# Optimization experiments

Hardware: AMD Instinct MI355X
Metric: run time of the kernel (lower is better)

Reference implementation:

```python
import jax, jax.numpy as jnp
import numpy as np

HEADS = 16
NUM_LANDMARKS = 64
PINV_ITERS = 6
D_MODEL = 1024


def _moore_penrose_pinv(x, num_iters):
    # Newton-Schulz iteration: V <- 0.25*V @ (13I - KV @ (15I - KV @ (7I - KV)))
    m = x.shape[-1]
    I = jnp.eye(m, dtype=x.dtype)
    V = x
    for _ in range(num_iters):
        KV = x @ V  # [..., m, m]
        V = 0.25 * V @ (13.0 * I - KV @ (15.0 * I - KV @ (7.0 * I - KV)))
    return V


def setup_inputs() -> dict:
    key = jax.random.key(0)
    k1, k2, k3 = jax.random.split(key, 3)
    b, n, d = 4, 4096, D_MODEL
    hidden_states = jax.random.normal(k1, (b, n, d), dtype=jnp.float32)
    Wqkv = jax.random.normal(k2, (d, 3 * d), dtype=jnp.float32) * 0.02
    bqkv = jnp.zeros((3 * d,), dtype=jnp.float32)
    Wout = jax.random.normal(k3, (d, d), dtype=jnp.float32) * 0.02
    bout = jnp.zeros((d,), dtype=jnp.float32)
    return {"hidden_states": hidden_states, "Wqkv": Wqkv, "bqkv": bqkv,
            "Wout": Wout, "bout": bout}


def reference(hidden_states, Wqkv, bqkv, Wout, bout):
    b, n, d = hidden_states.shape
    h, m = HEADS, NUM_LANDMARKS
    dh = d // h
    scale = 1.0 / np.sqrt(dh).astype(np.float32)
    # n is a multiple of m by construction, so the torch padding branch is a no-op.
    l = n // m  # tokens per landmark group

    qkv = hidden_states @ Wqkv + bqkv  # [b, n, 3d]
    q, k, v = jnp.split(qkv, 3, axis=-1)

    def to_heads(t):  # [b, n, d] -> [b, h, n, dh]
        return t.reshape(b, n, h, dh).transpose(0, 2, 1, 3)

    q, k, v = to_heads(q), to_heads(k), to_heads(v)
    q = q * scale

    # Landmarks: mean over contiguous groups of l tokens (sum / l in original).
    q_l = q.reshape(b, h, m, l, dh).mean(axis=3)  # [b, h, m, dh]
    k_l = k.reshape(b, h, m, l, dh).mean(axis=3)

    sim1 = jnp.einsum('bhid,bhjd->bhij', q, k_l)    # [b, h, n, m]
    sim2 = jnp.einsum('bhid,bhjd->bhij', q_l, k_l)  # [b, h, m, m]
    sim3 = jnp.einsum('bhid,bhjd->bhij', q_l, k)    # [b, h, m, n]

    attn1 = jax.nn.softmax(sim1, axis=-1)
    attn2 = jax.nn.softmax(sim2, axis=-1)
    attn3 = jax.nn.softmax(sim3, axis=-1)

    attn2_inv = _moore_penrose_pinv(attn2, PINV_ITERS)

    # out = attn1 @ attn2_inv @ (attn3 @ v), cheapest association
    out = attn1 @ (attn2_inv @ (attn3 @ v))  # [b, h, n, dh]
    out = out.transpose(0, 2, 1, 3).reshape(b, n, d)
    out = out @ Wout + bout
    return out
```

## Files before the change

### kernel.cpp

```cpp
#include <hip/hip_runtime.h>
#include <cstdint>

typedef unsigned short u16;
typedef __attribute__((ext_vector_type(8))) short s16x8;
typedef __attribute__((ext_vector_type(4))) float f32x4;

#define NTOK 4096
#define DH   64
#define DM   1024
#define NH   16

static __device__ __forceinline__ float b2f(u16 u){ return __uint_as_float(((unsigned)u)<<16); }
static __device__ __forceinline__ u16 f2b(float f){
  unsigned u = __float_as_uint(f);
  return (u16)((u + 0x7FFFu + ((u>>16)&1u)) >> 16);
}

static __device__ __forceinline__ void gload_lds16(const void* g, void* l) {
  __builtin_amdgcn_global_load_lds(
      (const __attribute__((address_space(1))) unsigned*)(uintptr_t)g,
      (__attribute__((address_space(3))) unsigned*)(uintptr_t)l, 16, 0, 0);
}

static __device__ __forceinline__ s16x8 ld8(const u16* p){ return *(const s16x8*)(const void*)p; }

__global__ __launch_bounds__(256) void k_cvt_xl(const float* __restrict__ hs, u16* __restrict__ Xb,
                                                float* __restrict__ Xl) {
  const int grp = blockIdx.x;
  const int d = blockIdx.y*256 + threadIdx.x;
  const float* p = hs + (long)grp*64*DM + d;
  u16* xo = Xb + (long)grp*64*DM + d;
  float s = 0.f;
  #pragma unroll 8
  for (int i = 0; i < 64; ++i) {
    const float v = p[(long)i*DM];
    s += v;
    xo[(long)i*DM] = f2b(v);
  }
  Xl[(long)grp*DM + d] = s * (1.0f/64.0f);
}

__global__ __launch_bounds__(256) void k_cvt_t(const float* __restrict__ in, u16* __restrict__ out, int R, int C) {
  __shared__ float tile[64][65];
  const int tc = blockIdx.x, tr = blockIdx.y;
  const int t = threadIdx.x, cx = t & 63, ry = t >> 6;
  #pragma unroll
  for (int p = 0; p < 16; ++p) {
    const int row = p*4 + ry;
    tile[row][cx] = in[(long)(tr*64 + row)*C + tc*64 + cx];
  }
  __syncthreads();
  #pragma unroll
  for (int p = 0; p < 16; ++p) {
    const int orow = p*4 + ry;
    out[(long)(tc*64 + orow)*R + tr*64 + cx] = f2b(tile[cx][orow]);
  }
}

__global__ __launch_bounds__(256) void k_lproj2(const float* __restrict__ Xl, const float* __restrict__ Wqkv,
                                                float* __restrict__ psum) {
  __shared__ __align__(16) float Xs[32][68];
  const int t = threadIdx.x;
  const int wcol = blockIdx.x*256 + t;
  const int r0 = blockIdx.y*32;
  const int kbase = blockIdx.z*128;
  float acc[32];
  #pragma unroll
  for (int r = 0; r < 32; ++r) acc[r] = 0.f;
  for (int k0 = kbase; k0 < kbase + 128; k0 += 64) {
    __syncthreads();
    for (int idx = t; idx < 2048; idx += 256)
      Xs[idx>>6][idx&63] = Xl[(long)(r0 + (idx>>6))*DM + k0 + (idx&63)];
    __syncthreads();
    for (int kk = 0; kk < 64; kk += 4) {
      f32x4 wv;
      #pragma unroll
      for (int j = 0; j < 4; ++j) wv[j] = Wqkv[(long)(k0+kk+j)*3072 + wcol];
      #pragma unroll
      for (int r = 0; r < 32; ++r) {
        const f32x4 xv = *(const f32x4*)&Xs[r][kk];
        acc[r] += xv[0]*wv[0] + xv[1]*wv[1] + xv[2]*wv[2] + xv[3]*wv[3];
      }
    }
  }
  float* po = psum + ((long)blockIdx.z*256 + r0)*2048 + wcol;
  #pragma unroll
  for (int r = 0; r < 32; ++r) po[(long)r*2048] = acc[r];
}

__global__ __launch_bounds__(256) void k_lreduce(const float* __restrict__ psum, const float* __restrict__ bqkv,
                                                 float* __restrict__ qlf, float* __restrict__ klf,
                                                 u16* __restrict__ qlb, u16* __restrict__ klb) {
  const long idx = (long)blockIdx.x*256 + threadIdx.x;
  const int row = (int)(idx >> 11), col = (int)(idx & 2047);
  float s = 0.f;
  #pragma unroll
  for (int z = 0; z < 8; ++z) s += psum[((long)z*256 + row)*2048 + col];
  const int isq = (col < 1024) ? 1 : 0;
  float val = s + bqkv[col];
  if (isq) val *= 0.125f;
  const int b = row >> 6, lm = row & 63;
  const int c2 = col & 1023, h = c2 >> 6, dh = c2 & 63;
  const long o = (((long)b*NH + h)*64 + lm)*64 + dh;
  if (isq) { qlf[o] = val; qlb[o] = f2b(val); }
  else     { klf[o] = val; klb[o] = f2b(val); }
}

template<int EPI>
__global__ __launch_bounds__(512, 2) void k_gemm256(
    const u16* __restrict__ A, const u16* __restrict__ Bt, const float* __restrict__ bias,
    int N, float* __restrict__ outF, u16* __restrict__ outQ, u16* __restrict__ outK, u16* __restrict__ outV)
{
  __shared__ __align__(16) u16 lds[4*16384];
  const int K = 1024;
  const int t = threadIdx.x;
  const int lane = t & 63;
  const int wid = t >> 6;
  const int c = lane & 15, g = lane >> 4;
  const int wm = wid >> 2, wn = wid & 3;
  const int fid = blockIdx.y*64 + blockIdx.x;
  const int nbx = ((fid & 7) << 3) | ((fid >> 3) & 7);
  const int nby = fid >> 6;
  const long arow0 = (long)nbx * 256;
  const long brow0 = (long)nby * 256;
  char* ldsb = (char*)lds;

  const int srow = t >> 2;
  const int schunk = (t & 3) ^ ((srow >> 1) & 3);
  const u16* gA0 = A  + (arow0 + srow)*K       + schunk*8;
  const u16* gA1 = A  + (arow0 + 128 + srow)*K + schunk*8;
  const u16* gB0 = Bt + (brow0 + srow)*K       + schunk*8;
  const u16* gB1 = Bt + (brow0 + 128 + srow)*K + schunk*8;
  const int dstoff = t*16;

#define STAGE_A(kt) { char* bse = ldsb + ((kt)&3)*32768; \
    gload_lds16(gA0 + (kt)*32, bse + dstoff); \
    gload_lds16(gA1 + (kt)*32, bse + 8192 + dstoff); }
#define STAGE_B(kt) { char* bse = ldsb + ((kt)&3)*32768 + 16384; \
    gload_lds16(gB0 + (kt)*32, bse + dstoff); \
    gload_lds16(gB1 + (kt)*32, bse + 8192 + dstoff); }

  const int gs = g ^ ((c >> 1) & 3);
  int aoff[2][4], boff[4];
  #pragma unroll
  for (int mi = 0; mi < 4; ++mi) {
    aoff[0][mi] = (0*128 + wm*64 + mi*16 + c)*64 + gs*16;
    aoff[1][mi] = (1*128 + wm*64 + mi*16 + c)*64 + gs*16;
    boff[mi]    = 16384 + (wn*64 + mi*16 + c)*64 + gs*16;
  }

  f32x4 acc0[4][4] = {};
  f32x4 acc1[4][4] = {};

  STAGE_A(0); STAGE_B(0); STAGE_A(1); STAGE_B(1); STAGE_A(2); STAGE_B(2);
  asm volatile("s_waitcnt vmcnt(8)" ::: "memory");
  __builtin_amdgcn_s_barrier();

  s16x8 af[4], bfr[4], af2[4];
  #pragma unroll
  for (int mi = 0; mi < 4; ++mi) af[mi]  = *(const s16x8*)(ldsb + aoff[0][mi]);
  #pragma unroll
  for (int ni = 0; ni < 4; ++ni) bfr[ni] = *(const s16x8*)(ldsb + boff[ni]);

  for (int kt = 0; kt < 32; ++kt) {
    char* buf  = ldsb + (kt&3)*32768;
    char* bufn = ldsb + ((kt+1)&3)*32768;
    if (kt + 3 < 32) { STAGE_A(kt+3) STAGE_B(kt+3) }
    asm volatile("s_waitcnt lgkmcnt(0)" ::: "memory");
    __builtin_amdgcn_sched_barrier(0);
    #pragma unroll
    for (int mi = 0; mi < 4; ++mi) af2[mi] = *(const s16x8*)(buf + aoff[1][mi]);
    __builtin_amdgcn_sched_barrier(0);
    __builtin_amdgcn_s_setprio(1);
    #pragma unroll
    for (int mi = 0; mi < 4; ++mi)
      #pragma unroll
      for (int ni = 0; ni < 4; ++ni)
        acc0[mi][ni] = __builtin_amdgcn_mfma_f32_16x16x32_bf16(af[mi], bfr[ni], acc0[mi][ni], 0, 0, 0);
    __builtin_amdgcn_s_setprio(0);
    asm volatile("s_waitcnt lgkmcnt(0)" ::: "memory");
    __builtin_amdgcn_sched_barrier(0);
    if (kt <= 28)      { asm volatile("s_waitcnt vmcnt(8)" ::: "memory"); }
    else if (kt == 29) { asm volatile("s_waitcnt vmcnt(4)" ::: "memory"); }
    else if (kt == 30) { asm volatile("s_waitcnt vmcnt(0)" ::: "memory"); }
    if (kt < 31) __builtin_amdgcn_s_barrier();
    s16x8 nf[4], nb[4];
    if (kt < 31) {
      #pragma unroll
      for (int mi = 0; mi < 4; ++mi) nf[mi] = *(const s16x8*)(bufn + aoff[0][mi]);
      #pragma unroll
      for (int ni = 0; ni < 4; ++ni) nb[ni] = *(const s16x8*)(bufn + boff[ni]);
    }
    __builtin_amdgcn_sched_barrier(0);
    __builtin_amdgcn_s_setprio(1);
    #pragma unroll
    for (int mi = 0; mi < 4; ++mi)
      #pragma unroll
      for (int ni = 0; ni < 4; ++ni)
        acc1[mi][ni] = __builtin_amdgcn_mfma_f32_16x16x32_bf16(af2[mi], bfr[ni], acc1[mi][ni], 0, 0, 0);
    __builtin_amdgcn_s_setprio(0);
    if (kt < 31) {
      #pragma unroll
      for (int mi = 0; mi < 4; ++mi) { af[mi] = nf[mi]; bfr[mi] = nb[mi]; }
    }
  }
#undef STAGE_A
#undef STAGE_B

  if (EPI == 0) {
    const int tensor = (int)(brow0 >> 10);
    u16* dst = (tensor == 0) ? outQ : (tensor == 1) ? outK : outV;
    const float mul = (tensor == 0) ? 0.125f : 1.0f;
    #pragma unroll
    for (int ph = 0; ph < 2; ++ph)
      #pragma unroll
      for (int mi = 0; mi < 4; ++mi) {
        const int rowb = ph*128 + wm*64 + mi*16 + g*4;
        #pragma unroll
        for (int ni = 0; ni < 4; ++ni) {
          const long gcol = brow0 + wn*64 + ni*16 + c;
          const int c2 = (int)(gcol & 1023);
          const int head = c2 >> 6, dh = c2 & 63;
          const float bv = bias[gcol];
          const f32x4 a = ph ? acc1[mi][ni] : acc0[mi][ni];
          #pragma unroll
          for (int r = 0; r < 4; ++r) {
            const long grow = arow0 + rowb + r;
            const int b = (int)(grow >> 12), tok = (int)(grow & 4095);
            dst[(((long)b*NH + head)*NTOK + tok)*DH + dh] = f2b((a[r] + bv)*mul);
          }
        }
      }
  } else {
    #pragma unroll
    for (int ph = 0; ph < 2; ++ph)
      #pragma unroll
      for (int mi = 0; mi < 4; ++mi) {
        const int rowb = ph*128 + wm*64 + mi*16 + g*4;
        #pragma unroll
        for (int ni = 0; ni < 4; ++ni) {
          const long gcol = brow0 + wn*64 + ni*16 + c;
          const float bv = bias[gcol];
          const f32x4 a = ph ? acc1[mi][ni] : acc0[mi][ni];
          #pragma unroll
          for (int r = 0; r < 4; ++r) {
            const long grow = arow0 + rowb + r;
            outF[grow*N + gcol] = a[r] + bv;
          }
        }
      }
  }
}

__global__ __launch_bounds__(256) void k_vtrans(const u16* __restrict__ v, u16* __restrict__ vt) {
  __shared__ u16 tile[64][65];
  const int bh = blockIdx.x >> 6, tt = blockIdx.x & 63;
  const int t = threadIdx.x, cx = t & 63, ry = t >> 6;
  const u16* vp = v + ((long)bh*NTOK + tt*64)*DH;
  #pragma unroll
  for (int p = 0; p < 16; ++p) { const int row = p*4 + ry; tile[row][cx] = vp[row*DH + cx]; }
  __syncthreads();
  u16* op = vt + (long)bh*DH*NTOK + tt*64;
  #pragma unroll
  for (int p = 0; p < 16; ++p) { const int orow = p*4 + ry; op[(long)orow*NTOK + cx] = tile[cx][orow]; }
}

#define PST 68
static __device__ __forceinline__ void mm_nn8(const float* A, const float* B, float* C, int t) {
  const int lane = t & 63, j0 = (t >> 6) << 3;
  float acc[8];
  #pragma unroll
  for (int j = 0; j < 8; ++j) acc[j] = 0.f;
  for (int k = 0; k < 64; k += 4) {
    const f32x4 a4 = *(const f32x4*)&A[lane*PST + k];
    #pragma unroll
    for (int dk = 0; dk < 4; ++dk) {
      const float a = a4[dk];
      const float* br = &B[(k + dk)*PST + j0];
      const f32x4 b0 = *(const f32x4*)(br);
      const f32x4 b1 = *(const f32x4*)(br + 4);
      #pragma unroll
      for (int qq = 0; qq < 4; ++qq) { acc[qq] += a*b0[qq]; acc[4+qq] += a*b1[qq]; }
    }
  }
  #pragma unroll
  for (int j = 0; j < 8; ++j) C[lane*PST + j0 + j] = acc[j];
}
static __device__ __forceinline__ void mm_nt8(const float* A, const float* B, float* C, int t) {
  const int lane = t & 63, j0 = (t >> 6) << 3;
  float acc[8];
  #pragma unroll
  for (int j = 0; j < 8; ++j) acc[j] = 0.f;
  for (int k = 0; k < 64; k += 4) {
    const f32x4 a4 = *(const f32x4*)&A[lane*PST + k];
    #pragma unroll
    for (int jj = 0; jj < 8; ++jj) {
      const f32x4 b4 = *(const f32x4*)&B[(j0 + jj)*PST + k];
      acc[jj] += a4[0]*b4[0] + a4[1]*b4[1] + a4[2]*b4[2] + a4[3]*b4[3];
    }
  }
  #pragma unroll
  for (int j = 0; j < 8; ++j) C[lane*PST + j0 + j] = acc[j];
}

__global__ __launch_bounds__(512) void k_pinv(const float* __restrict__ qlf, const float* __restrict__ klf,
                                              float* __restrict__ a2inv) {
  __shared__ __align__(16) float Xb[64*PST];
  __shared__ __align__(16) float Vb[64*PST];
  __shared__ __align__(16) float T1[64*PST];
  __shared__ __align__(16) float T2[64*PST];
  __shared__ __align__(16) float T3[64*PST];
  const int bh = blockIdx.x, t = threadIdx.x;
  const float* ql = qlf + (long)bh*4096;
  const float* kl = klf + (long)bh*4096;
  for (int i = t; i < 4096; i += 512) { T1[(i>>6)*PST + (i&63)] = ql[i]; T2[(i>>6)*PST + (i&63)] = kl[i]; }
  __syncthreads();
  mm_nt8(T1, T2, Xb, t);
  __syncthreads();
  if (t < 64) {
    float mx = -1e30f;
    for (int j = 0; j < 64; ++j) mx = fmaxf(mx, Xb[t*PST + j]);
    float s = 0.f;
    for (int j = 0; j < 64; ++j) { const float e = expf(Xb[t*PST + j] - mx); Xb[t*PST + j] = e; s += e; }
    const float inv = 1.0f/s;
    for (int j = 0; j < 64; ++j) Xb[t*PST + j] *= inv;
  }
  __syncthreads();
  for (int i = t; i < 4096; i += 512) { const int r = i>>6, cc = i&63; Vb[r*PST+cc] = Xb[r*PST+cc]; }
  __syncthreads();
  for (int it = 0; it < 6; ++it) {
    mm_nn8(Xb, Vb, T1, t);  __syncthreads();
    for (int i = t; i < 4096; i += 512) { const int r=i>>6, cc=i&63; T2[r*PST+cc] = (r==cc?7.0f:0.0f) - T1[r*PST+cc]; }
    __syncthreads();
    mm_nn8(T1, T2, T3, t);  __syncthreads();
    for (int i = t; i < 4096; i += 512) { const int r=i>>6, cc=i&63; T2[r*PST+cc] = (r==cc?15.0f:0.0f) - T3[r*PST+cc]; }
    __syncthreads();
    mm_nn8(T1, T2, T3, t);  __syncthreads();
    for (int i = t; i < 4096; i += 512) { const int r=i>>6, cc=i&63; T2[r*PST+cc] = (r==cc?13.0f:0.0f) - T3[r*PST+cc]; }
    __syncthreads();
    mm_nn8(Vb, T2, T3, t);  __syncthreads();
    for (int i = t; i < 4096; i += 512) { const int r=i>>6, cc=i&63; Vb[r*PST+cc] = 0.25f*T3[r*PST+cc]; }
    __syncthreads();
  }
  for (int i = t; i < 4096; i += 512) a2inv[(long)bh*4096 + i] = Vb[(i>>6)*PST + (i&63)];
}

__global__ __launch_bounds__(256) void k_attn3v_p(const u16* __restrict__ qlb, const u16* __restrict__ kk,
                                                  const u16* __restrict__ vt,
                                                  float* __restrict__ zp, float* __restrict__ sp) {
  __shared__ __align__(16) float Zl[4][64][64];
  __shared__ float Sl[4][64];
  __shared__ __align__(16) u16 Pl[4][64][40];
  const int bh = blockIdx.x >> 2, qt = blockIdx.x & 3;
  const int t = threadIdx.x, w = t >> 6, lane = t & 63;
  const int c = lane & 15, g = lane >> 4;

  s16x8 aq[4][2];
  const u16* qlp = qlb + (long)bh*4096;
  #pragma unroll
  for (int mi = 0; mi < 4; ++mi)
    #pragma unroll
    for (int ks = 0; ks < 2; ++ks)
      aq[mi][ks] = ld8(qlp + (mi*16 + c)*64 + ks*32 + g*8);

  f32x4 zacc[4][4] = {};
  float sl[4][4] = {};
  const u16* kp = kk + (long)bh*NTOK*DH;
  const u16* vp = vt + (long)bh*DH*NTOK;
  char* pbase = (char*)&Pl[w][0][0];
  const int tok00 = qt*1024 + w*256;

  for (int it = 0; it < 8; ++it) {
    const int t0 = tok00 + it*32;
    f32x4 sacc[4][2] = {};
    s16x8 kb[2][2];
    #pragma unroll
    for (int cg = 0; cg < 2; ++cg)
      #pragma unroll
      for (int ks = 0; ks < 2; ++ks)
        kb[cg][ks] = ld8(kp + (long)(t0 + cg*16 + c)*64 + ks*32 + g*8);
    #pragma unroll
    for (int cg = 0; cg < 2; ++cg)
      #pragma unroll
      for (int ks = 0; ks < 2; ++ks)
        #pragma unroll
        for (int mi = 0; mi < 4; ++mi)
          sacc[mi][cg] = __builtin_amdgcn_mfma_f32_16x16x32_bf16(aq[mi][ks], kb[cg][ks], sacc[mi][cg], 0, 0, 0);
    #pragma unroll
    for (int mi = 0; mi < 4; ++mi)
      #pragma unroll
      for (int r = 0; r < 4; ++r) {
        const int row = mi*16 + g*4 + r;
        const float p0 = __expf(sacc[mi][0][r]);
        const float p1 = __expf(sacc[mi][1][r]);
        sl[mi][r] += p0 + p1;
        char* base = pbase + row*80;
        *(u16*)(base + c*2)      = f2b(p0);
        *(u16*)(base + 32 + c*2) = f2b(p1);
      }
    s16x8 pa[4];
    #pragma unroll
    for (int mi = 0; mi < 4; ++mi) pa[mi] = *(const s16x8*)(pbase + (mi*16 + c)*80 + g*16);
    #pragma unroll
    for (int ni = 0; ni < 4; ++ni) {
      const s16x8 vb = ld8(vp + (long)(ni*16 + c)*NTOK + t0 + g*8);
      #pragma unroll
      for (int mi = 0; mi < 4; ++mi)
        zacc[mi][ni] = __builtin_amdgcn_mfma_f32_16x16x32_bf16(pa[mi], vb, zacc[mi][ni], 0, 0, 0);
    }
  }
  #pragma unroll
  for (int mi = 0; mi < 4; ++mi)
    #pragma unroll
    for (int r = 0; r < 4; ++r) {
      float s = sl[mi][r];
      s += __shfl_xor(s, 1); s += __shfl_xor(s, 2); s += __shfl_xor(s, 4); s += __shfl_xor(s, 8);
      sl[mi][r] = s;
    }
  #pragma unroll
  for (int mi = 0; mi < 4; ++mi)
    #pragma unroll
    for (int ni = 0; ni < 4; ++ni)
      #pragma unroll
      for (int r = 0; r < 4; ++r)
        Zl[w][mi*16 + g*4 + r][ni*16 + c] = zacc[mi][ni][r];
  if (c == 0)
    #pragma unroll
    for (int mi = 0; mi < 4; ++mi)
      #pragma unroll
      for (int r = 0; r < 4; ++r)
        Sl[w][mi*16 + g*4 + r] = sl[mi][r];
  __syncthreads();
  float* zpp = zp + (long)blockIdx.x*4096;
  for (int i = t; i < 4096; i += 256) {
    const int row = i >> 6, dh = i & 63;
    zpp[i] = Zl[0][row][dh] + Zl[1][row][dh] + Zl[2][row][dh] + Zl[3][row][dh];
  }
  if (t < 64) sp[(long)blockIdx.x*64 + t] = Sl[0][t] + Sl[1][t] + Sl[2][t] + Sl[3][t];
}

__global__ __launch_bounds__(512) void k_w2(const float* __restrict__ a2inv,
                                            const float* __restrict__ zp, const float* __restrict__ sp,
                                            u16* __restrict__ w2t) {
  __shared__ __align__(16) float Ai[64*PST];
  __shared__ __align__(16) float Zi[64*PST];
  __shared__ __align__(16) float Ci[64*PST];
  __shared__ float Ss[64];
  const int bh = blockIdx.x, t = threadIdx.x;
  if (t < 64) {
    float ss = 0.f;
    #pragma unroll
    for (int qt = 0; qt < 4; ++qt) ss += sp[(long)(bh*4 + qt)*64 + t];
    Ss[t] = 1.0f / ss;
  }
  for (int i = t; i < 4096; i += 512)
    Ai[(i>>6)*PST + (i&63)] = a2inv[(long)bh*4096 + i];
  __syncthreads();
  for (int i = t; i < 4096; i += 512) {
    float zs = 0.f;
    #pragma unroll
    for (int qt = 0; qt < 4; ++qt) zs += zp[((long)(bh*4 + qt))*4096 + i];
    Zi[(i>>6)*PST + (i&63)] = zs * Ss[i>>6];
  }
  __syncthreads();
  mm_nn8(Ai, Zi, Ci, t);
  __syncthreads();
  for (int i = t; i < 4096; i += 512) { const int r = i>>6, cc = i&63; w2t[(long)bh*4096 + cc*64 + r] = f2b(Ci[r*PST + cc]); }
}

#define P1ST 144
__global__ __launch_bounds__(256) void k_attn1(const u16* __restrict__ q, const u16* __restrict__ klb,
                                               const u16* __restrict__ w2t, u16* __restrict__ ao) {
  __shared__ __align__(16) u16 Pl[4][64][72];
  const int bx = blockIdx.x, bh = bx >> 4, tt = bx & 15;
  const int b = bh >> 4, h = bh & 15;
  const int t = threadIdx.x, w = t >> 6, lane = t & 63;
  const int c = lane & 15, g = lane >> 4;
  const int tok0 = tt*256 + w*64;
  const u16* qp  = q + ((long)bh*NTOK + tok0)*DH;
  const u16* klp = klb + (long)bh*4096;
  const u16* wp  = w2t + (long)bh*4096;
  char* pbase = (char*)&Pl[w][0][0];

  s16x8 aq[4][2], kb[4][2], wb[4][2];
  #pragma unroll
  for (int i = 0; i < 4; ++i)
    #pragma unroll
    for (int ks = 0; ks < 2; ++ks) {
      aq[i][ks] = ld8(qp + (long)(i*16 + c)*DH + ks*32 + g*8);
      kb[i][ks] = ld8(klp + (i*16 + c)*64 + ks*32 + g*8);
      wb[i][ks] = ld8(wp  + (i*16 + c)*64 + ks*32 + g*8);
    }
  f32x4 sacc[4][4] = {};
  #pragma unroll
  for (int ks = 0; ks < 2; ++ks)
    #pragma unroll
    for (int mi = 0; mi < 4; ++mi)
      #pragma unroll
      for (int ni = 0; ni < 4; ++ni)
        sacc[mi][ni] = __builtin_amdgcn_mfma_f32_16x16x32_bf16(aq[mi][ks], kb[ni][ks], sacc[mi][ni], 0, 0, 0);

  float rs[4][4];
  #pragma unroll
  for (int mi = 0; mi < 4; ++mi)
    #pragma unroll
    for (int r = 0; r < 4; ++r) {
      const int row = mi*16 + g*4 + r;
      char* base = pbase + row*P1ST;
      float ssum = 0.f;
      #pragma unroll
      for (int ni = 0; ni < 4; ++ni) {
        const float p = __expf(sacc[mi][ni][r]);
        ssum += p;
        *(u16*)(base + (ni*16 + c)*2) = f2b(p);
      }
      ssum += __shfl_xor(ssum, 1); ssum += __shfl_xor(ssum, 2);
      ssum += __shfl_xor(ssum, 4); ssum += __shfl_xor(ssum, 8);
      rs[mi][r] = ssum;
    }
  __builtin_amdgcn_s_barrier();
  s16x8 pa[4][2];
  #pragma unroll
  for (int mi = 0; mi < 4; ++mi)
    #pragma unroll
    for (int ks = 0; ks < 2; ++ks)
      pa[mi][ks] = *(const s16x8*)(pbase + (mi*16 + c)*P1ST + ks*64 + g*16);
  f32x4 oacc[4][4] = {};
  #pragma unroll
  for (int ks = 0; ks < 2; ++ks)
    #pragma unroll
    for (int mi = 0; mi < 4; ++mi)
      #pragma unroll
      for (int ni = 0; ni < 4; ++ni)
        oacc[mi][ni] = __builtin_amdgcn_mfma_f32_16x16x32_bf16(pa[mi][ks], wb[ni][ks], oacc[mi][ni], 0, 0, 0);

  u16* op = ao + (long)b*NTOK*DM + (long)h*64;
  #pragma unroll
  for (int mi = 0; mi < 4; ++mi)
    #pragma unroll
    for (int r = 0; r < 4; ++r) {
      const int tok = tok0 + mi*16 + g*4 + r;
      const float inv = 1.0f / rs[mi][r];
      #pragma unroll
      for (int ni = 0; ni < 4; ++ni)
        op[(long)tok*DM + ni*16 + c] = f2b(oacc[mi][ni][r] * inv);
    }
}

extern "C" void kernel_launch(void* const* d_in, const int* in_sizes, int n_in,
                              void* d_out, int out_size, void* d_ws, size_t ws_size,
                              hipStream_t stream) {
  const float* hs   = (const float*)d_in[0];
  const float* Wqkv = (const float*)d_in[1];
  const float* bqkv = (const float*)d_in[2];
  const float* Wout = (const float*)d_in[3];
  const float* bout = (const float*)d_in[4];
  float* out = (float*)d_out;
  char* w = (char*)d_ws;

  u16*  Xb    = (u16*)(w);
  float* zp   = (float*)(w);
  float* sp   = (float*)(w + 4194304L);
  u16*  WqkvT = (u16*)(w + 33554432L);
  u16*  WoutT = (u16*)(w + 39845888L);
  u16*  q     = (u16*)(w + 41943040L);
  float* psum = (float*)(w + 41943040L);
  u16*  k     = (u16*)(w + 75497472L);
  u16*  v     = (u16*)(w + 109051904L);
  u16*  vt    = (u16*)(w + 142606336L);
  float* Xl   = (float*)(w + 142606336L);
  float* qlf  = (float*)(w + 176160768L);
  float* klf  = (float*)(w + 177209344L);
  u16*  qlb   = (u16*)(w + 178257920L);
  u16*  klb   = (u16*)(w + 178782208L);
  float* a2i  = (float*)(w + 179306496L);
  u16*  w2t   = (u16*)(w + 181403648L);
  u16*  ao    = (u16*)(w + 181927936L);

  k_cvt_xl<<<dim3(256,4), 256, 0, stream>>>(hs, Xb, Xl);
  k_cvt_t<<<dim3(48,16), 256, 0, stream>>>(Wqkv, WqkvT, 1024, 3072);
  k_cvt_t<<<dim3(16,16), 256, 0, stream>>>(Wout, WoutT, 1024, 1024);
  k_lproj2<<<dim3(8,8,8), 256, 0, stream>>>(Xl, Wqkv, psum);
  k_lreduce<<<2048, 256, 0, stream>>>(psum, bqkv, qlf, klf, qlb, klb);
  k_gemm256<0><<<dim3(64,12), 512, 0, stream>>>(Xb, WqkvT, bqkv, 3072, nullptr, q, k, v);
  k_vtrans<<<4096, 256, 0, stream>>>(v, vt);
  k_pinv<<<64, 512, 0, stream>>>(qlf, klf, a2i);
  k_attn3v_p<<<256, 256, 0, stream>>>(qlb, k, vt, zp, sp);
  k_w2<<<64, 512, 0, stream>>>(a2i, zp, sp, w2t);
  k_attn1<<<1024, 256, 0, stream>>>(q, klb, w2t, ao);
  k_gemm256<1><<<dim3(64,4), 512, 0, stream>>>(ao, WoutT, bout, 1024, out, nullptr, nullptr, nullptr);
}
```

Before: 367.6 us.

## Fuse V transpose into QKV GEMM, restage GEMM loop, widen pinv/attn3 parallelism

```diff
diff --git a/kernel.cpp b/kernel.cpp
--- a/kernel.cpp
+++ b/kernel.cpp
@@ -133,12 +133,10 @@
   const u16* gB1 = Bt + (brow0 + 128 + srow)*K + schunk*8;
   const int dstoff = t*16;
 
-#define STAGE_A(kt) { char* bse = ldsb + ((kt)&3)*32768; \
-    gload_lds16(gA0 + (kt)*32, bse + dstoff); \
-    gload_lds16(gA1 + (kt)*32, bse + 8192 + dstoff); }
-#define STAGE_B(kt) { char* bse = ldsb + ((kt)&3)*32768 + 16384; \
-    gload_lds16(gB0 + (kt)*32, bse + dstoff); \
-    gload_lds16(gB1 + (kt)*32, bse + 8192 + dstoff); }
+#define GL_A0(kt) gload_lds16(gA0 + (kt)*32, ldsb + ((kt)&3)*32768 + dstoff);
+#define GL_A1(kt) gload_lds16(gA1 + (kt)*32, ldsb + ((kt)&3)*32768 + 8192 + dstoff);
+#define GL_B0(kt) gload_lds16(gB0 + (kt)*32, ldsb + ((kt)&3)*32768 + 16384 + dstoff);
+#define GL_B1(kt) gload_lds16(gB1 + (kt)*32, ldsb + ((kt)&3)*32768 + 24576 + dstoff);
 
   const int gs = g ^ ((c >> 1) & 3);
   int aoff[2][4], boff[4];
@@ -152,85 +150,129 @@
   f32x4 acc0[4][4] = {};
   f32x4 acc1[4][4] = {};
 
-  STAGE_A(0); STAGE_B(0); STAGE_A(1); STAGE_B(1); STAGE_A(2); STAGE_B(2);
+  GL_A0(0) GL_A1(0) GL_B0(0) GL_B1(0)
+  GL_A0(1) GL_A1(1) GL_B0(1) GL_B1(1)
+  GL_A0(2) GL_A1(2) GL_B0(2) GL_B1(2)
   asm volatile("s_waitcnt vmcnt(8)" ::: "memory");
   __builtin_amdgcn_s_barrier();
 
-  s16x8 af[4], bfr[4], af2[4];
-  #pragma unroll
-  for (int mi = 0; mi < 4; ++mi) af[mi]  = *(const s16x8*)(ldsb + aoff[0][mi]);
-  #pragma unroll
-  for (int ni = 0; ni < 4; ++ni) bfr[ni] = *(const s16x8*)(ldsb + boff[ni]);
-
   for (int kt = 0; kt < 32; ++kt) {
-    char* buf  = ldsb + (kt&3)*32768;
-    char* bufn = ldsb + ((kt+1)&3)*32768;
-    if (kt + 3 < 32) { STAGE_A(kt+3) STAGE_B(kt+3) }
+    char* buf = ldsb + (kt&3)*32768;
+    s16x8 fa0, fa1, fb[4];
+    if (kt + 3 < 32) GL_A0(kt+3)
+    fa0 = *(const s16x8*)(buf + aoff[0][0]);
+    fa1 = *(const s16x8*)(buf + aoff[0][1]);
+    #pragma unroll
+    for (int ni = 0; ni < 4; ++ni) fb[ni] = *(const s16x8*)(buf + boff[ni]);
     asm volatile("s_waitcnt lgkmcnt(0)" ::: "memory");
     __builtin_amdgcn_sched_barrier(0);
-    #pragma unroll
-    for (int mi = 0; mi < 4; ++mi) af2[mi] = *(const s16x8*)(buf + aoff[1][mi]);
+    __builtin_amdgcn_s_setprio(1);
+    #pragma unroll
+    for (int ni = 0; ni < 4; ++ni) acc0[0][ni] = __builtin_amdgcn_mfma_f32_16x16x32_bf16(fa0, fb[ni], acc0[0][ni], 0, 0, 0);
+    #pragma unroll
+    for (int ni = 0; ni < 4; ++ni) acc0[1][ni] = __builtin_amdgcn_mfma_f32_16x16x32_bf16(fa1, fb[ni], acc0[1][ni], 0, 0, 0);
+    __builtin_amdgcn_s_setprio(0);
+    if (kt + 3 < 32) GL_A1(kt+3)
+    fa0 = *(const s16x8*)(buf + aoff[0][2]);
+    fa1 = *(const s16x8*)(buf + aoff[0][3]);
+    asm volatile("s_waitcnt lgkmcnt(0)" ::: "memory");
     __builtin_amdgcn_sched_barrier(0);
     __builtin_amdgcn_s_setprio(1);
     #pragma unroll
-    for (int mi = 0; mi < 4; ++mi)
-      #pragma unroll
-      for (int ni = 0; ni < 4; ++ni)
-        acc0[mi][ni] = __builtin_amdgcn_mfma_f32_16x16x32_bf16(af[mi], bfr[ni], acc0[mi][ni], 0, 0, 0);
+    for (int ni = 0; ni < 4; ++ni) acc0[2][ni] = __builtin_amdgcn_mfma_f32_16x16x32_bf16(fa0, fb[ni], acc0[2][ni], 0, 0, 0);
+    #pragma unroll
+    for (int ni = 0; ni < 4; ++ni) acc0[3][ni] = __builtin_amdgcn_mfma_f32_16x16x32_bf16(fa1, fb[ni], acc0[3][ni], 0, 0, 0);
     __builtin_amdgcn_s_setprio(0);
+    if (kt + 3 < 32) GL_B0(kt+3)
+    fa0 = *(const s16x8*)(buf + aoff[1][0]);
+    fa1 = *(const s16x8*)(buf + aoff[1][1]);
     asm volatile("s_waitcnt lgkmcnt(0)" ::: "memory");
     __builtin_amdgcn_sched_barrier(0);
+    __builtin_amdgcn_s_setprio(1);
+    #pragma unroll
+    for (int ni = 0; ni < 4; ++ni) acc1[0][ni] = __builtin_amdgcn_mfma_f32_16x16x32_bf16(fa0, fb[ni], acc1[0][ni], 0, 0, 0);
+    #pragma unroll
+    for (int ni = 0; ni < 4; ++ni) acc1[1][ni] = __builtin_amdgcn_mfma_f32_16x16x32_bf16(fa1, fb[ni], acc1[1][ni], 0, 0, 0);
+    __builtin_amdgcn_s_setprio(0);
+    if (kt + 3 < 32) GL_B1(kt+3)
+    fa0 = *(const s16x8*)(buf + aoff[1][2]);
+    fa1 = *(const s16x8*)(buf + aoff[1][3]);
+    asm volatile("s_waitcnt lgkmcnt(0)" ::: "memory");
+    __builtin_amdgcn_sched_barrier(0);
+    __builtin_amdgcn_s_setprio(1);
+    #pragma unroll
+    for (int ni = 0; ni < 4; ++ni) acc1[2][ni] = __builtin_amdgcn_mfma_f32_16x16x32_bf16(fa0, fb[ni], acc1[2][ni], 0, 0, 0);
+    #pragma unroll
+    for (int ni = 0; ni < 4; ++ni) acc1[3][ni] = __builtin_amdgcn_mfma_f32_16x16x32_bf16(fa1, fb[ni], acc1[3][ni], 0, 0, 0);
+    __builtin_amdgcn_s_setprio(0);
     if (kt <= 28)      { asm volatile("s_waitcnt vmcnt(8)" ::: "memory"); }
     else if (kt == 29) { asm volatile("s_waitcnt vmcnt(4)" ::: "memory"); }
     else if (kt == 30) { asm volatile("s_waitcnt vmcnt(0)" ::: "memory"); }
-    if (kt < 31) __builtin_amdgcn_s_barrier();
-    s16x8 nf[4], nb[4];
-    if (kt < 31) {
-      #pragma unroll
-      for (int mi = 0; mi < 4; ++mi) nf[mi] = *(const s16x8*)(bufn + aoff[0][mi]);
-      #pragma unroll
-      for (int ni = 0; ni < 4; ++ni) nb[ni] = *(const s16x8*)(bufn + boff[ni]);
-    }
-    __builtin_amdgcn_sched_barrier(0);
-    __builtin_amdgcn_s_setprio(1);
-    #pragma unroll
-    for (int mi = 0; mi < 4; ++mi)
-      #pragma unroll
-      for (int ni = 0; ni < 4; ++ni)
-        acc1[mi][ni] = __builtin_amdgcn_mfma_f32_16x16x32_bf16(af2[mi], bfr[ni], acc1[mi][ni], 0, 0, 0);
-    __builtin_amdgcn_s_setprio(0);
-    if (kt < 31) {
-      #pragma unroll
-      for (int mi = 0; mi < 4; ++mi) { af[mi] = nf[mi]; bfr[mi] = nb[mi]; }
-    }
-  }
-#undef STAGE_A
-#undef STAGE_B
+    __builtin_amdgcn_s_barrier();
+  }
+#undef GL_A0
+#undef GL_A1
+#undef GL_B0
+#undef GL_B1
 
   if (EPI == 0) {
     const int tensor = (int)(brow0 >> 10);
-    u16* dst = (tensor == 0) ? outQ : (tensor == 1) ? outK : outV;
-    const float mul = (tensor == 0) ? 0.125f : 1.0f;
-    #pragma unroll
-    for (int ph = 0; ph < 2; ++ph)
-      #pragma unroll
-      for (int mi = 0; mi < 4; ++mi) {
-        const int rowb = ph*128 + wm*64 + mi*16 + g*4;
+    if (tensor == 2) {
+      __syncthreads();
+      u16* wlds = lds + wid*4224;
+      const int hbase = (int)((brow0 + wn*64) & 1023);
+      const int head = hbase >> 6;
+      #pragma unroll
+      for (int ph = 0; ph < 2; ++ph) {
+        const long grow0 = arow0 + ph*128 + wm*64;
+        const int b = (int)(grow0 >> 12), tok0r = (int)(grow0 & 4095);
         #pragma unroll
-        for (int ni = 0; ni < 4; ++ni) {
-          const long gcol = brow0 + wn*64 + ni*16 + c;
-          const int c2 = (int)(gcol & 1023);
-          const int head = c2 >> 6, dh = c2 & 63;
-          const float bv = bias[gcol];
-          const f32x4 a = ph ? acc1[mi][ni] : acc0[mi][ni];
+        for (int mi = 0; mi < 4; ++mi)
           #pragma unroll
-          for (int r = 0; r < 4; ++r) {
-            const long grow = arow0 + rowb + r;
-            const int b = (int)(grow >> 12), tok = (int)(grow & 4095);
-            dst[(((long)b*NH + head)*NTOK + tok)*DH + dh] = f2b((a[r] + bv)*mul);
+          for (int ni = 0; ni < 4; ++ni) {
+            const float bv = bias[brow0 + wn*64 + ni*16 + c];
+            const f32x4 a = ph ? acc1[mi][ni] : acc0[mi][ni];
+            #pragma unroll
+            for (int r = 0; r < 4; ++r)
+              wlds[(mi*16 + g*4 + r)*66 + ni*16 + c] = f2b(a[r] + bv);
+          }
+        asm volatile("s_waitcnt lgkmcnt(0)" ::: "memory");
+        u16* vbase = outV + (((long)b*NH + head)*DH)*NTOK + tok0r;
+        #pragma unroll
+        for (int j = 0; j < 8; ++j) {
+          const int d = j*8 + (lane >> 3);
+          const int tk = (lane & 7)*8;
+          s16x8 vv;
+          #pragma unroll
+          for (int s2 = 0; s2 < 8; ++s2) vv[s2] = (short)wlds[(tk + s2)*66 + d];
+          *(s16x8*)(vbase + (long)d*NTOK + tk) = vv;
+        }
+        asm volatile("s_waitcnt lgkmcnt(0)" ::: "memory");
+      }
+    } else {
+      u16* dst = (tensor == 0) ? outQ : outK;
+      const float mul = (tensor == 0) ? 0.125f : 1.0f;
+      #pragma unroll
+      for (int ph = 0; ph < 2; ++ph)
+        #pragma unroll
+        for (int mi = 0; mi < 4; ++mi) {
+          const int rowb = ph*128 + wm*64 + mi*16 + g*4;
+          #pragma unroll
+          for (int ni = 0; ni < 4; ++ni) {
+            const long gcol = brow0 + wn*64 + ni*16 + c;
+            const int c2 = (int)(gcol & 1023);
+            const int head = c2 >> 6, dh = c2 & 63;
+            const float bv = bias[gcol];
+            const f32x4 a = ph ? acc1[mi][ni] : acc0[mi][ni];
+            #pragma unroll
+            for (int r = 0; r < 4; ++r) {
+              const long grow = arow0 + rowb + r;
+              const int b = (int)(grow >> 12), tok = (int)(grow & 4095);
+              dst[(((long)b*NH + head)*NTOK + tok)*DH + dh] = f2b((a[r] + bv)*mul);
+            }
           }
         }
-      }
+    }
   } else {
     #pragma unroll
     for (int ph = 0; ph < 2; ++ph)
@@ -252,59 +294,39 @@
   }
 }
 
-__global__ __launch_bounds__(256) void k_vtrans(const u16* __restrict__ v, u16* __restrict__ vt) {
-  __shared__ u16 tile[64][65];
-  const int bh = blockIdx.x >> 6, tt = blockIdx.x & 63;
-  const int t = threadIdx.x, cx = t & 63, ry = t >> 6;
-  const u16* vp = v + ((long)bh*NTOK + tt*64)*DH;
-  #pragma unroll
-  for (int p = 0; p < 16; ++p) { const int row = p*4 + ry; tile[row][cx] = vp[row*DH + cx]; }
-  __syncthreads();
-  u16* op = vt + (long)bh*DH*NTOK + tt*64;
-  #pragma unroll
-  for (int p = 0; p < 16; ++p) { const int orow = p*4 + ry; op[(long)orow*NTOK + cx] = tile[cx][orow]; }
-}
-
 #define PST 68
-static __device__ __forceinline__ void mm_nn8(const float* A, const float* B, float* C, int t) {
-  const int lane = t & 63, j0 = (t >> 6) << 3;
-  float acc[8];
-  #pragma unroll
-  for (int j = 0; j < 8; ++j) acc[j] = 0.f;
+static __device__ __forceinline__ void mm_nn4(const float* A, const float* B, float* C, int t) {
+  const int lane = t & 63, j0 = (t >> 6) << 2;
+  float acc[4] = {0.f, 0.f, 0.f, 0.f};
   for (int k = 0; k < 64; k += 4) {
     const f32x4 a4 = *(const f32x4*)&A[lane*PST + k];
     #pragma unroll
     for (int dk = 0; dk < 4; ++dk) {
-      const float a = a4[dk];
-      const float* br = &B[(k + dk)*PST + j0];
-      const f32x4 b0 = *(const f32x4*)(br);
-      const f32x4 b1 = *(const f32x4*)(br + 4);
-      #pragma unroll
-      for (int qq = 0; qq < 4; ++qq) { acc[qq] += a*b0[qq]; acc[4+qq] += a*b1[qq]; }
-    }
-  }
-  #pragma unroll
-  for (int j = 0; j < 8; ++j) C[lane*PST + j0 + j] = acc[j];
-}
-static __device__ __forceinline__ void mm_nt8(const float* A, const float* B, float* C, int t) {
-  const int lane = t & 63, j0 = (t >> 6) << 3;
-  float acc[8];
-  #pragma unroll
-  for (int j = 0; j < 8; ++j) acc[j] = 0.f;
+      const f32x4 b0 = *(const f32x4*)&B[(k + dk)*PST + j0];
+      #pragma unroll
+      for (int q = 0; q < 4; ++q) acc[q] += a4[dk]*b0[q];
+    }
+  }
+  #pragma unroll
+  for (int j = 0; j < 4; ++j) C[lane*PST + j0 + j] = acc[j];
+}
+static __device__ __forceinline__ void mm_nt4(const float* A, const float* B, float* C, int t) {
+  const int lane = t & 63, j0 = (t >> 6) << 2;
+  float acc[4] = {0.f, 0.f, 0.f, 0.f};
   for (int k = 0; k < 64; k += 4) {
     const f32x4 a4 = *(const f32x4*)&A[lane*PST + k];
     #pragma unroll
-    for (int jj = 0; jj < 8; ++jj) {
+    for (int jj = 0; jj < 4; ++jj) {
       const f32x4 b4 = *(const f32x4*)&B[(j0 + jj)*PST + k];
       acc[jj] += a4[0]*b4[0] + a4[1]*b4[1] + a4[2]*b4[2] + a4[3]*b4[3];
     }
   }
   #pragma unroll
-  for (int j = 0; j < 8; ++j) C[lane*PST + j0 + j] = acc[j];
-}
-
-__global__ __launch_bounds__(512) void k_pinv(const float* __restrict__ qlf, const float* __restrict__ klf,
-                                              float* __restrict__ a2inv) {
+  for (int j = 0; j < 4; ++j) C[lane*PST + j0 + j] = acc[j];
+}
+
+__global__ __launch_bounds__(1024) void k_pinv(const float* __restrict__ qlf, const float* __restrict__ klf,
+                                               float* __restrict__ a2inv) {
   __shared__ __align__(16) float Xb[64*PST];
   __shared__ __align__(16) float Vb[64*PST];
   __shared__ __align__(16) float T1[64*PST];
@@ -313,9 +335,9 @@
   const int bh = blockIdx.x, t = threadIdx.x;
   const float* ql = qlf + (long)bh*4096;
   const float* kl = klf + (long)bh*4096;
-  for (int i = t; i < 4096; i += 512) { T1[(i>>6)*PST + (i&63)] = ql[i]; T2[(i>>6)*PST + (i&63)] = kl[i]; }
-  __syncthreads();
-  mm_nt8(T1, T2, Xb, t);
+  for (int i = t; i < 4096; i += 1024) { T1[(i>>6)*PST + (i&63)] = ql[i]; T2[(i>>6)*PST + (i&63)] = kl[i]; }
+  __syncthreads();
+  mm_nt4(T1, T2, Xb, t);
   __syncthreads();
   if (t < 64) {
     float mx = -1e30f;
@@ -326,23 +348,23 @@
     for (int j = 0; j < 64; ++j) Xb[t*PST + j] *= inv;
   }
   __syncthreads();
-  for (int i = t; i < 4096; i += 512) { const int r = i>>6, cc = i&63; Vb[r*PST+cc] = Xb[r*PST+cc]; }
+  for (int i = t; i < 4096; i += 1024) { const int r = i>>6, cc = i&63; Vb[r*PST+cc] = Xb[r*PST+cc]; }
   __syncthreads();
   for (int it = 0; it < 6; ++it) {
-    mm_nn8(Xb, Vb, T1, t);  __syncthreads();
-    for (int i = t; i < 4096; i += 512) { const int r=i>>6, cc=i&63; T2[r*PST+cc] = (r==cc?7.0f:0.0f) - T1[r*PST+cc]; }
+    mm_nn4(Xb, Vb, T1, t);  __syncthreads();
+    for (int i = t; i < 4096; i += 1024) { const int r=i>>6, cc=i&63; T2[r*PST+cc] = (r==cc?7.0f:0.0f) - T1[r*PST+cc]; }
     __syncthreads();
-    mm_nn8(T1, T2, T3, t);  __syncthreads();
-    for (int i = t; i < 4096; i += 512) { const int r=i>>6, cc=i&63; T2[r*PST+cc] = (r==cc?15.0f:0.0f) - T3[r*PST+cc]; }
+    mm_nn4(T1, T2, T3, t);  __syncthreads();
+    for (int i = t; i < 4096; i += 1024) { const int r=i>>6, cc=i&63; T2[r*PST+cc] = (r==cc?15.0f:0.0f) - T3[r*PST+cc]; }
     __syncthreads();
-    mm_nn8(T1, T2, T3, t);  __syncthreads();
-    for (int i = t; i < 4096; i += 512) { const int r=i>>6, cc=i&63; T2[r*PST+cc] = (r==cc?13.0f:0.0f) - T3[r*PST+cc]; }
+    mm_nn4(T1, T2, T3, t);  __syncthreads();
+    for (int i = t; i < 4096; i += 1024) { const int r=i>>6, cc=i&63; T2[r*PST+cc] = (r==cc?13.0f:0.0f) - T3[r*PST+cc]; }
     __syncthreads();
-    mm_nn8(Vb, T2, T3, t);  __syncthreads();
-    for (int i = t; i < 4096; i += 512) { const int r=i>>6, cc=i&63; Vb[r*PST+cc] = 0.25f*T3[r*PST+cc]; }
+    mm_nn4(Vb, T2, T3, t);  __syncthreads();
+    for (int i = t; i < 4096; i += 1024) { const int r=i>>6, cc=i&63; Vb[r*PST+cc] = 0.25f*T3[r*PST+cc]; }
     __syncthreads();
   }
-  for (int i = t; i < 4096; i += 512) a2inv[(long)bh*4096 + i] = Vb[(i>>6)*PST + (i&63)];
+  for (int i = t; i < 4096; i += 1024) a2inv[(long)bh*4096 + i] = Vb[(i>>6)*PST + (i&63)];
 }
 
 __global__ __launch_bounds__(256) void k_attn3v_p(const u16* __restrict__ qlb, const u16* __restrict__ kk,
@@ -351,7 +373,7 @@
   __shared__ __align__(16) float Zl[4][64][64];
   __shared__ float Sl[4][64];
   __shared__ __align__(16) u16 Pl[4][64][40];
-  const int bh = blockIdx.x >> 2, qt = blockIdx.x & 3;
+  const int bh = blockIdx.x >> 3, qt = blockIdx.x & 7;
   const int t = threadIdx.x, w = t >> 6, lane = t & 63;
   const int c = lane & 15, g = lane >> 4;
 
@@ -368,9 +390,9 @@
   const u16* kp = kk + (long)bh*NTOK*DH;
   const u16* vp = vt + (long)bh*DH*NTOK;
   char* pbase = (char*)&Pl[w][0][0];
-  const int tok00 = qt*1024 + w*256;
-
-  for (int it = 0; it < 8; ++it) {
+  const int tok00 = qt*512 + w*128;
+
+  for (int it = 0; it < 4; ++it) {
     const int t0 = tok00 + it*32;
     f32x4 sacc[4][2] = {};
     s16x8 kb[2][2];
@@ -439,9 +461,9 @@
   if (t < 64) sp[(long)blockIdx.x*64 + t] = Sl[0][t] + Sl[1][t] + Sl[2][t] + Sl[3][t];
 }
 
-__global__ __launch_bounds__(512) void k_w2(const float* __restrict__ a2inv,
-                                            const float* __restrict__ zp, const float* __restrict__ sp,
-                                            u16* __restrict__ w2t) {
+__global__ __launch_bounds__(1024) void k_w2(const float* __restrict__ a2inv,
+                                             const float* __restrict__ zp, const float* __restrict__ sp,
+                                             u16* __restrict__ w2t) {
   __shared__ __align__(16) float Ai[64*PST];
   __shared__ __align__(16) float Zi[64*PST];
   __shared__ __align__(16) float Ci[64*PST];
@@ -450,22 +472,22 @@
   if (t < 64) {
     float ss = 0.f;
     #pragma unroll
-    for (int qt = 0; qt < 4; ++qt) ss += sp[(long)(bh*4 + qt)*64 + t];
+    for (int qt = 0; qt < 8; ++qt) ss += sp[(long)(bh*8 + qt)*64 + t];
     Ss[t] = 1.0f / ss;
   }
-  for (int i = t; i < 4096; i += 512)
+  for (int i = t; i < 4096; i += 1024)
     Ai[(i>>6)*PST + (i&63)] = a2inv[(long)bh*4096 + i];
   __syncthreads();
-  for (int i = t; i < 4096; i += 512) {
+  for (int i = t; i < 4096; i += 1024) {
     float zs = 0.f;
     #pragma unroll
-    for (int qt = 0; qt < 4; ++qt) zs += zp[((long)(bh*4 + qt))*4096 + i];
+    for (int qt = 0; qt < 8; ++qt) zs += zp[((long)(bh*8 + qt))*4096 + i];
     Zi[(i>>6)*PST + (i&63)] = zs * Ss[i>>6];
   }
   __syncthreads();
-  mm_nn8(Ai, Zi, Ci, t);
-  __syncthreads();
-  for (int i = t; i < 4096; i += 512) { const int r = i>>6, cc = i&63; w2t[(long)bh*4096 + cc*64 + r] = f2b(Ci[r*PST + cc]); }
+  mm_nn4(Ai, Zi, Ci, t);
+  __syncthreads();
+  for (int i = t; i < 4096; i += 1024) { const int r = i>>6, cc = i&63; w2t[(long)bh*4096 + cc*64 + r] = f2b(Ci[r*PST + cc]); }
 }
 
 #define P1ST 144
@@ -560,15 +582,14 @@
 
   u16*  Xb    = (u16*)(w);
   float* zp   = (float*)(w);
-  float* sp   = (float*)(w + 4194304L);
+  float* sp   = (float*)(w + 8388608L);
   u16*  WqkvT = (u16*)(w + 33554432L);
   u16*  WoutT = (u16*)(w + 39845888L);
   u16*  q     = (u16*)(w + 41943040L);
   float* psum = (float*)(w + 41943040L);
   u16*  k     = (u16*)(w + 75497472L);
-  u16*  v     = (u16*)(w + 109051904L);
   u16*  vt    = (u16*)(w + 142606336L);
-  float* Xl   = (float*)(w + 142606336L);
+  float* Xl   = (float*)(w + 109051904L);
   float* qlf  = (float*)(w + 176160768L);
   float* klf  = (float*)(w + 177209344L);
   u16*  qlb   = (u16*)(w + 178257920L);
@@ -582,11 +603,10 @@
   k_cvt_t<<<dim3(16,16), 256, 0, stream>>>(Wout, WoutT, 1024, 1024);
   k_lproj2<<<dim3(8,8,8), 256, 0, stream>>>(Xl, Wqkv, psum);
   k_lreduce<<<2048, 256, 0, stream>>>(psum, bqkv, qlf, klf, qlb, klb);
-  k_gemm256<0><<<dim3(64,12), 512, 0, stream>>>(Xb, WqkvT, bqkv, 3072, nullptr, q, k, v);
-  k_vtrans<<<4096, 256, 0, stream>>>(v, vt);
-  k_pinv<<<64, 512, 0, stream>>>(qlf, klf, a2i);
-  k_attn3v_p<<<256, 256, 0, stream>>>(qlb, k, vt, zp, sp);
-  k_w2<<<64, 512, 0, stream>>>(a2i, zp, sp, w2t);
+  k_gemm256<0><<<dim3(64,12), 512, 0, stream>>>(Xb, WqkvT, bqkv, 3072, nullptr, q, k, vt);
+  k_pinv<<<64, 1024, 0, stream>>>(qlf, klf, a2i);
+  k_attn3v_p<<<512, 256, 0, stream>>>(qlb, k, vt, zp, sp);
+  k_w2<<<64, 1024, 0, stream>>>(a2i, zp, sp, w2t);
   k_attn1<<<1024, 256, 0, stream>>>(q, klb, w2t, ao);
   k_gemm256<1><<<dim3(64,4), 512, 0, stream>>>(ao, WoutT, bout, 1024, out, nullptr, nullptr, nullptr);
 }
```

New measurement: 356.5 us. 3.0% less time.
